# Optimization experiments

Hardware: AMD Instinct MI355X
Metric: run time of the kernel (lower is better)

Reference implementation:

```python
import jax, jax.numpy as jnp
import numpy as np

B, S, DM = 1, 4096, 2048
H, HD = 16, 128
TS = 16          # tile_size
TOPK = 16        # anchor tiles per query
NUM_TILES = S // TS


def setup_inputs() -> dict:
    key = jax.random.key(0)
    ks = jax.random.split(key, 7)
    x = jax.random.normal(ks[0], (B, S, DM), jnp.float32)
    Wq = jax.random.normal(ks[1], (DM, H * HD), jnp.float32) * 0.02
    Wk = jax.random.normal(ks[2], (DM, H * HD), jnp.float32) * 0.02
    Wv = jax.random.normal(ks[3], (DM, H * HD), jnp.float32) * 0.02
    Wo = jax.random.normal(ks[4], (H * HD, DM), jnp.float32) * 0.02
    # RoPE angles: pos * inv_freq, shape [S, HD//2] (= freqs_cis angle)
    inv_freq = 1.0 / (10000.0 ** (np.arange(0, HD, 2, dtype=np.float32) / HD))
    freqs = jnp.asarray(np.arange(S, dtype=np.float32)[:, None] * inv_freq[None, :])
    anchor_indices = jax.random.randint(ks[5], (B, H, S, TOPK), 0, NUM_TILES).astype(jnp.int32)
    return {"x": x, "Wq": Wq, "Wk": Wk, "Wv": Wv, "Wo": Wo,
            "freqs": freqs, "anchor_indices": anchor_indices}


def _rotate_half(z):
    half = z.shape[-1] // 2
    return jnp.concatenate([-z[..., half:], z[..., :half]], axis=-1)


def reference(x, Wq, Wk, Wv, Wo, freqs, anchor_indices):
    b, s, _ = x.shape
    num_tiles = s // TS
    # QKV projections -> [B, H, S, HD]
    q = (x @ Wq).reshape(b, s, H, HD).transpose(0, 2, 1, 3)
    k = (x @ Wk).reshape(b, s, H, HD).transpose(0, 2, 1, 3)
    v = (x @ Wv).reshape(b, s, H, HD).transpose(0, 2, 1, 3)
    # RoPE (half-split / rotate_half convention), float32
    cos = jnp.cos(freqs)[None, None, :s, :]
    sin = jnp.sin(freqs)[None, None, :s, :]
    cos_full = jnp.concatenate([cos, cos], axis=-1)
    sin_full = jnp.concatenate([sin, sin], axis=-1)
    q = q * cos_full + _rotate_half(q) * sin_full
    k = k * cos_full + _rotate_half(k) * sin_full
    # Per-query tile indices: anchor tiles + local tile
    local_tiles = (jnp.arange(s) // TS).astype(jnp.int32)
    local = jnp.broadcast_to(local_tiles[None, None, :, None], (b, H, s, 1))
    tiles = jnp.concatenate([anchor_indices, local], axis=-1)  # [B,H,S,K+1]
    # Representative query per tile (last token of each query tile)
    tile_repr = jnp.arange(TS - 1, s, TS)
    tile_sel = tiles[:, :, tile_repr, :]                        # [B,H,T,K+1]
    # Expand tile indices to token indices
    offsets = jnp.arange(TS)
    token_idx = tile_sel[..., None] * TS + offsets              # [B,H,T,K+1,TS]
    sparse_len = tile_sel.shape[-1] * TS
    flat_idx = jnp.clip(token_idx.reshape(b, H, num_tiles, sparse_len), 0, s - 1)
    # Gather sparse K/V per (batch, head, query-tile)
    k_flat = k.reshape(b * H, s, HD)
    v_flat = v.reshape(b * H, s, HD)
    idx_flat = flat_idx.reshape(b * H, num_tiles, sparse_len)
    k_sparse = jax.vmap(lambda kv, idx: kv[idx])(k_flat, idx_flat)
    v_sparse = jax.vmap(lambda kv, idx: kv[idx])(v_flat, idx_flat)
    k_sparse = k_sparse.reshape(b, H, num_tiles, sparse_len, HD)
    v_sparse = v_sparse.reshape(b, H, num_tiles, sparse_len, HD)
    # Block-sparse attention per tile
    q_tiled = q.reshape(b, H, num_tiles, TS, HD)
    logits = jnp.einsum('bhtqd,bhtkd->bhtqk', q_tiled, k_sparse) / jnp.sqrt(HD)
    q_pos = jnp.arange(s).reshape(num_tiles, TS)
    future_mask = flat_idx[:, :, :, None, :] > q_pos[None, None, :, :, None]
    logits = jnp.where(future_mask, -1e10, logits)
    weights = jax.nn.softmax(logits, axis=-1)
    all_masked = jnp.all(future_mask, axis=-1, keepdims=True)
    weights = jnp.where(all_masked, 0.0, weights)
    weights = jnp.where(jnp.isnan(weights), 0.0, weights)
    out = jnp.einsum('bhtqk,bhtkd->bhtqd', weights, v_sparse)
    out = out.reshape(b, H, s, HD).transpose(0, 2, 1, 3).reshape(b, s, H * HD)
    return out @ Wo
```

## Files before the change

kernel.cpp:

```cpp
#include <hip/hip_runtime.h>

typedef unsigned short u16;
typedef unsigned int u32;
typedef __attribute__((ext_vector_type(8))) short bf16x8;
typedef __attribute__((ext_vector_type(4))) float f32x4;

__device__ __forceinline__ u16 f2bf(float f) {
  union { float f; u32 u; } v; v.f = f;
  u32 u = v.u;
  return (u16)((u + 0x7FFFu + ((u >> 16) & 1u)) >> 16);
}
__device__ __forceinline__ float bf2f(u16 s) {
  union { u32 u; float f; } v; v.u = ((u32)s) << 16;
  return v.f;
}

__device__ __forceinline__ void async16(const void* g, void* l) {
  __builtin_amdgcn_global_load_lds(
      (__attribute__((address_space(1))) void*)g,
      (__attribute__((address_space(3))) void*)l, 16, 0, 0);
}

__global__ void prep1_kernel(const float* __restrict__ x,
                             const float* __restrict__ W0, const float* __restrict__ W1,
                             const float* __restrict__ W2, const float* __restrict__ W3,
                             const float* __restrict__ freqs,
                             u16* __restrict__ xbf, u16* __restrict__ wqkvT,
                             u16* __restrict__ woT,
                             float* __restrict__ ct, float* __restrict__ st) {
  __shared__ float tile[64][33];
  const int bid = blockIdx.x;
  const int tid = threadIdx.x;
  if (bid < 8192) {
    const int z = bid >> 11;
    const float* in = z == 0 ? W0 : z == 1 ? W1 : z == 2 ? W2 : W3;
    u16* out = z == 3 ? woT : wqkvT + (size_t)z * 4194304;
    const int local = bid & 2047;
    const int c0 = (local & 63) * 32;
    const int r0 = (local >> 6) * 64;
#pragma unroll
    for (int it = 0; it < 8; ++it) {
      int idx = it * 256 + tid;
      int row = idx >> 5, col = idx & 31;
      tile[row][col] = in[(size_t)(r0 + row) * 2048 + c0 + col];
    }
    __syncthreads();
#pragma unroll
    for (int it = 0; it < 4; ++it) {
      int idx = it * 256 + tid;
      int orow = idx >> 5, oc2 = idx & 31;
      u32 v = (u32)f2bf(tile[2 * oc2][orow]) | ((u32)f2bf(tile[2 * oc2 + 1][orow]) << 16);
      *(u32*)(out + (size_t)(c0 + orow) * 2048 + r0 + 2 * oc2) = v;
    }
  } else if (bid < 16384) {
    int i = (bid - 8192) * 256 + tid;
    float4 v = ((const float4*)x)[i];
    ushort4 o;
    o.x = f2bf(v.x); o.y = f2bf(v.y); o.z = f2bf(v.z); o.w = f2bf(v.w);
    ((ushort4*)xbf)[i] = o;
  } else {
    int i = (bid - 16384) * 256 + tid;
    float f = freqs[i];
    ct[i] = cosf(f); st[i] = sinf(f);
  }
}

template <int MODE>
__launch_bounds__(256, 3)
__global__ void gemm128_kernel(const u16* __restrict__ A, const u16* __restrict__ Bt,
                               void* __restrict__ C, u16* __restrict__ D1, u16* __restrict__ D2,
                               const float* __restrict__ ct, const float* __restrict__ st,
                               int M, int N, int K) {
  __shared__ __align__(16) char smem[33152];
  u16* As = (u16*)smem;
  u16* Bs = (u16*)(smem + 16384);
  const int tid  = threadIdx.x;
  const int lane = tid & 63;
  const int wave = tid >> 6;
  const int wr = wave >> 1, wc = wave & 1;
  const int g = lane >> 4, c = lane & 15;
  const int brow = blockIdx.y * 128;
  const int bcol = blockIdx.x * 128;

  int a_goff[4], b_goff[4], l_off[4];
#pragma unroll
  for (int i = 0; i < 4; ++i) {
    int p = (wave * 4 + i) * 1024 + lane * 16;
    int row = p >> 7;
    int colb = (p & 127) ^ ((row & 7) << 4);
    a_goff[i] = (brow + row) * K + (colb >> 1);
    b_goff[i] = (bcol + row) * K + (colb >> 1);
    l_off[i] = p;
  }

  f32x4 acc[4][4];
#pragma unroll
  for (int m = 0; m < 4; ++m)
#pragma unroll
    for (int n = 0; n < 4; ++n) acc[m][n] = (f32x4){0.f, 0.f, 0.f, 0.f};

  for (int k0 = 0; k0 < K; k0 += 64) {
#pragma unroll
    for (int i = 0; i < 4; ++i) {
      async16(A + a_goff[i] + k0, (char*)As + l_off[i]);
      async16(Bt + b_goff[i] + k0, (char*)Bs + l_off[i]);
    }
    __syncthreads();
#pragma unroll
    for (int kk = 0; kk < 2; ++kk) {
      bf16x8 af[4], bfr[4];
#pragma unroll
      for (int m = 0; m < 4; ++m) {
        int row = wr * 64 + m * 16 + c;
        int byte = (row << 7) + ((kk * 64 + (g << 4)) ^ ((row & 7) << 4));
        af[m] = *(const bf16x8*)((const char*)As + byte);
      }
#pragma unroll
      for (int n = 0; n < 4; ++n) {
        int row = ((n & 2) << 5) + wc * 32 + ((n & 1) << 4) + c;
        int byte = (row << 7) + ((kk * 64 + (g << 4)) ^ ((row & 7) << 4));
        bfr[n] = *(const bf16x8*)((const char*)Bs + byte);
      }
#pragma unroll
      for (int m = 0; m < 4; ++m)
#pragma unroll
        for (int n = 0; n < 4; ++n)
          acc[m][n] = __builtin_amdgcn_mfma_f32_16x16x32_bf16(af[m], bfr[n], acc[m][n], 0, 0, 0);
    }
    __syncthreads();
  }

  if (MODE == 2) {
    const int sel = bcol >> 11;
    const int hh  = (bcol & 2047) >> 7;
    if (sel < 2) {
#pragma unroll
      for (int m = 0; m < 4; ++m)
#pragma unroll
        for (int r = 0; r < 4; ++r) {
          const int t = brow + wr * 64 + m * 16 + g * 4 + r;
          const int tb = t * 64;
#pragma unroll
          for (int n = 0; n < 2; ++n) {
            const int d = wc * 32 + (n << 4) + c;
            float cv = ct[tb + d], sv = st[tb + d];
            float a = acc[m][n][r], b = acc[m][n + 2][r];
            u16 lo = f2bf(a * cv - b * sv);
            u16 hi = f2bf(b * cv + a * sv);
            if (sel == 0) {
              u16* qd = (u16*)C + (size_t)t * 2048 + hh * 128 + d;
              qd[0] = lo; qd[64] = hi;
            } else {
              u16* kd = D1 + ((size_t)hh * 4096 + t) * 128 + d;
              kd[0] = lo; kd[64] = hi;
            }
          }
        }
    } else {
      float* ep = (float*)smem;
#pragma unroll
      for (int half = 0; half < 2; ++half) {
        if (wr == half) {
#pragma unroll
          for (int m = 0; m < 4; ++m)
#pragma unroll
            for (int n = 0; n < 4; ++n)
#pragma unroll
              for (int r = 0; r < 4; ++r) {
                int lr = m * 16 + g * 4 + r;
                int lc = ((n & 2) << 5) + wc * 32 + ((n & 1) << 4) + c;
                ep[lr * 129 + lc] = acc[m][n][r];
              }
        }
        __syncthreads();
        const int rowbase = brow + half * 64;
#pragma unroll
        for (int it = 0; it < 16; ++it) {
          int idx = it * 256 + tid;
          int tl = idx >> 10;
          int d  = (idx >> 3) & 127;
          int k2 = idx & 7;
          u32 lo = f2bf(ep[(tl * 16 + 2 * k2) * 129 + d]);
          u32 hi = f2bf(ep[(tl * 16 + 2 * k2 + 1) * 129 + d]);
          int tile = (rowbase >> 4) + tl;
          *(u32*)(D2 + (((size_t)(hh * 256 + tile) * 128 + d) * 16 + 2 * k2)) = lo | (hi << 16);
        }
        __syncthreads();
      }
    }
  } else {
    const int r0 = brow + wr * 64;
#pragma unroll
    for (int m = 0; m < 4; ++m)
#pragma unroll
      for (int n = 0; n < 4; ++n)
#pragma unroll
        for (int r = 0; r < 4; ++r) {
          int rr = r0 + m * 16 + g * 4 + r;
          int cc = bcol + ((n & 2) << 5) + wc * 32 + ((n & 1) << 4) + c;
          ((float*)C)[(size_t)rr * N + cc] = acc[m][n][r];
        }
  }
}

__launch_bounds__(256, 6)
__global__ void attn_kernel(const u16* __restrict__ Q, const u16* __restrict__ Kp,
                            const u16* __restrict__ VT2, const int* __restrict__ anchors,
                            u16* __restrict__ Out) {
  const int t = blockIdx.x;
  const int h = blockIdx.y;
  __shared__ int tiles[20];
  __shared__ __align__(16) float lg[16][292];
  const int tid  = threadIdx.x;
  const int lane = tid & 63;
  const int wave = tid >> 6;
  const int g = lane >> 4;
  const int c = lane & 15;

  if (tid < 16) tiles[tid] = anchors[(size_t)((h << 12) + (t * 16 + 15)) * 16 + tid];
  if (tid == 16) tiles[16] = t;
  if (tid >= 17 && tid < 20) tiles[tid] = 0;
  __syncthreads();

  {
    const u16* qbase = Q + (size_t)(t * 16 + c) * 2048 + h * 128 + g * 8;
    bf16x8 qf[4];
#pragma unroll
    for (int ks = 0; ks < 4; ++ks) qf[ks] = *(const bf16x8*)(qbase + ks * 32);

    int tok_[5];
    const u16* kb_[5];
#pragma unroll
    for (int i = 0; i < 5; ++i) {
      int j = wave + 4 * i;
      tok_[i] = tiles[j] * 16 + c;
      kb_[i] = Kp + ((size_t)h * 4096 + tok_[i]) * 128 + g * 8;
    }
    bf16x8 kfp[2][4];
#pragma unroll
    for (int ks = 0; ks < 4; ++ks) kfp[0][ks] = *(const bf16x8*)(kb_[0] + ks * 32);
#pragma unroll
    for (int i = 0; i < 5; ++i) {
      if (i < 4) {
#pragma unroll
        for (int ks = 0; ks < 4; ++ks)
          kfp[(i + 1) & 1][ks] = *(const bf16x8*)(kb_[i + 1] + ks * 32);
      }
      f32x4 a = (f32x4){0.f, 0.f, 0.f, 0.f};
#pragma unroll
      for (int ks = 0; ks < 4; ++ks)
        a = __builtin_amdgcn_mfma_f32_16x16x32_bf16(qf[ks], kfp[i & 1][ks], a, 0, 0, 0);
      int j = wave + 4 * i;
      if (j < 17) {
#pragma unroll
        for (int r = 0; r < 4; ++r) {
          int qrow = g * 4 + r;
          float vv = a[r] * 0.088388347648318447f;
          if (tok_[i] > t * 16 + qrow) vv = -1e10f;
          lg[qrow][j * 16 + c] = vv;
        }
      }
    }
  }
  __syncthreads();

  {
    const int r = tid >> 4, cc = tid & 15;
    float vals[17];
    float mx = -3.0e38f;
#pragma unroll
    for (int i = 0; i < 17; ++i) { vals[i] = lg[r][i * 16 + cc]; mx = fmaxf(mx, vals[i]); }
#pragma unroll
    for (int d = 1; d < 16; d <<= 1) mx = fmaxf(mx, __shfl_xor(mx, d, 64));
    float sum = 0.f;
#pragma unroll
    for (int i = 0; i < 17; ++i) { vals[i] = __expf(vals[i] - mx); sum += vals[i]; }
#pragma unroll
    for (int d = 1; d < 16; d <<= 1) sum += __shfl_xor(sum, d, 64);
    float inv = sum > 0.f ? 1.0f / sum : 0.f;
    u16* wrow = (u16*)&lg[r][0];
#pragma unroll
    for (int i = 0; i < 17; ++i) wrow[i * 16 + cc] = f2bf(vals[i] * inv);
    wrow[272 + cc] = 0;
  }
  __syncthreads();

  {
    f32x4 o0 = (f32x4){0.f, 0.f, 0.f, 0.f}, o1 = o0;
    const int d0 = wave * 32;
    const size_t hb = (size_t)h * 256;
    const int keyin = (g & 1) * 8;
    const u16* wrow = (const u16*)&lg[c][0];
    const u16* vb_[9];
#pragma unroll
    for (int ks = 0; ks < 9; ++ks) vb_[ks] = VT2 + (hb + tiles[2 * ks + (g >> 1)]) * 2048;
    bf16x8 pb0[2], pb1[2];
    pb0[0] = *(const bf16x8*)(vb_[0] + (d0 + c) * 16 + keyin);
    pb1[0] = *(const bf16x8*)(vb_[0] + (d0 + 16 + c) * 16 + keyin);
#pragma unroll
    for (int ks = 0; ks < 9; ++ks) {
      if (ks < 8) {
        pb0[(ks + 1) & 1] = *(const bf16x8*)(vb_[ks + 1] + (d0 + c) * 16 + keyin);
        pb1[(ks + 1) & 1] = *(const bf16x8*)(vb_[ks + 1] + (d0 + 16 + c) * 16 + keyin);
      }
      bf16x8 af = *(const bf16x8*)(wrow + ks * 32 + g * 8);
      o0 = __builtin_amdgcn_mfma_f32_16x16x32_bf16(af, pb0[ks & 1], o0, 0, 0, 0);
      o1 = __builtin_amdgcn_mfma_f32_16x16x32_bf16(af, pb1[ks & 1], o1, 0, 0, 0);
    }
#pragma unroll
    for (int r = 0; r < 4; ++r) {
      int qrow = g * 4 + r;
      size_t base = (size_t)(t * 16 + qrow) * 2048 + h * 128;
      Out[base + d0 + c]      = f2bf(o0[r]);
      Out[base + d0 + 16 + c] = f2bf(o1[r]);
    }
  }
}

extern "C" void kernel_launch(void* const* d_in, const int* in_sizes, int n_in,
                              void* d_out, int out_size, void* d_ws, size_t ws_size,
                              hipStream_t stream) {
  (void)in_sizes; (void)n_in; (void)out_size; (void)ws_size;
  const float* x      = (const float*)d_in[0];
  const float* Wq     = (const float*)d_in[1];
  const float* Wk     = (const float*)d_in[2];
  const float* Wv     = (const float*)d_in[3];
  const float* Wo     = (const float*)d_in[4];
  const float* freqs  = (const float*)d_in[5];
  const int* anchors  = (const int*)d_in[6];
  float* out = (float*)d_out;

  char* ws = (char*)d_ws;
  const size_t MB = 1024 * 1024;
  u16* xbf   = (u16*)(ws + 0);
  u16* wqkvT = (u16*)(ws + 16 * MB);
  u16* woT   = (u16*)(ws + 40 * MB);
  u16* qbf   = (u16*)(ws + 48 * MB);
  u16* Kp    = (u16*)(ws + 64 * MB);
  u16* VT2   = (u16*)(ws + 80 * MB);
  u16* attnb = (u16*)(ws + 0);
  float* ct  = (float*)(ws + 96 * MB);
  float* st  = (float*)(ws + 97 * MB);

  prep1_kernel<<<17408, 256, 0, stream>>>(x, Wq, Wk, Wv, Wo, freqs,
                                          xbf, wqkvT, woT, ct, st);
  gemm128_kernel<2><<<dim3(48, 32), 256, 0, stream>>>(xbf, wqkvT, qbf, Kp, VT2,
                                                      ct, st, 4096, 6144, 2048);
  attn_kernel<<<dim3(256, 16), 256, 0, stream>>>(qbf, Kp, VT2, anchors, attnb);
  gemm128_kernel<0><<<dim3(16, 32), 256, 0, stream>>>(attnb, woT, out, nullptr, nullptr,
                                                      nullptr, nullptr, 4096, 2048, 2048);
}
```

Baseline: 226.6 us.

## Replace QKV GEMM with 256x256 double-buffered 8-wave pipelined kernel

The QKV projection GEMM moves from 128x128 tiles with a single LDS stage to 256x256 tiles with 512 threads and two 64KB LDS stages. Global-to-LDS async loads are interleaved with LDS fragment loads and MFMA blocks, using explicit vmcnt/lgkmcnt waits, raw barriers and s_setprio around the MFMA bursts. The goal is to hide load latency and raise operand reuse. The V-transpose epilogue now stages bf16 in shared memory instead of fp32, and the Wo GEMM is split into its own kernel with a simpler column mapping. The trade-off is one block per CU and a grid of only 384 blocks, which risks poor occupancy and a tail effect.

```diff
diff --git a/kernel.cpp b/kernel.cpp
--- a/kernel.cpp
+++ b/kernel.cpp
@@ -20,6 +20,12 @@
       (__attribute__((address_space(1))) void*)g,
       (__attribute__((address_space(3))) void*)l, 16, 0, 0);
 }
+
+#define VM4  asm volatile("s_waitcnt vmcnt(4)" ::: "memory")
+#define VM0  asm volatile("s_waitcnt vmcnt(0)" ::: "memory")
+#define LG0  asm volatile("s_waitcnt lgkmcnt(0)" ::: "memory")
+#define BARX do { asm volatile("" ::: "memory"); __builtin_amdgcn_s_barrier(); \
+                  asm volatile("" ::: "memory"); } while (0)
 
 __global__ void prep1_kernel(const float* __restrict__ x,
                              const float* __restrict__ W0, const float* __restrict__ W1,
@@ -65,15 +71,186 @@
   }
 }
 
-template <int MODE>
-__launch_bounds__(256, 3)
-__global__ void gemm128_kernel(const u16* __restrict__ A, const u16* __restrict__ Bt,
-                               void* __restrict__ C, u16* __restrict__ D1, u16* __restrict__ D2,
-                               const float* __restrict__ ct, const float* __restrict__ st,
-                               int M, int N, int K) {
-  __shared__ __align__(16) char smem[33152];
-  u16* As = (u16*)smem;
-  u16* Bs = (u16*)(smem + 16384);
+__launch_bounds__(512, 1)
+__global__ void gemm256_qkv_kernel(const u16* __restrict__ A, const u16* __restrict__ Bt,
+                                   u16* __restrict__ Q, u16* __restrict__ Kp,
+                                   u16* __restrict__ VT2,
+                                   const float* __restrict__ ct, const float* __restrict__ st) {
+  const int K = 2048;
+  __shared__ __align__(16) char smem[131072];
+  const int tid = threadIdx.x;
+  const int lane = tid & 63, wave = tid >> 6;
+  const int wm = wave >> 2, wn = wave & 3;
+  const int g = lane >> 4, c = lane & 15;
+  const int brow = blockIdx.y * 256;
+  const int bcol = blockIdx.x * 256;
+
+  int sp[2][2], aso[2][2], bso[2][2];
+#pragma unroll
+  for (int h = 0; h < 2; ++h)
+#pragma unroll
+    for (int cc = 0; cc < 2; ++cc) {
+      int p = h * 16384 + cc * 8192 + tid * 16;
+      int row = p >> 7;
+      int colb = (p & 127) ^ ((row & 7) << 4);
+      sp[h][cc] = p;
+      aso[h][cc] = (brow + row) * K + (colb >> 1);
+      bso[h][cc] = (bcol + row) * K + (colb >> 1);
+    }
+  auto stA = [&](int s, int h, int kt) {
+#pragma unroll
+    for (int cc = 0; cc < 2; ++cc)
+      async16(A + aso[h][cc] + kt * 64, smem + s * 65536 + sp[h][cc]);
+  };
+  auto stB = [&](int s, int h, int kt) {
+#pragma unroll
+    for (int cc = 0; cc < 2; ++cc)
+      async16(Bt + bso[h][cc] + kt * 64, smem + s * 65536 + 32768 + sp[h][cc]);
+  };
+
+  f32x4 acc[8][4];
+#pragma unroll
+  for (int m = 0; m < 8; ++m)
+#pragma unroll
+    for (int n = 0; n < 4; ++n) acc[m][n] = (f32x4){0.f, 0.f, 0.f, 0.f};
+  bf16x8 aF[4][2], bF[4][2];
+
+  auto LDA = [&](int s, int mh) {
+#pragma unroll
+    for (int mm = 0; mm < 4; ++mm) {
+      int row = wm * 128 + mh * 64 + mm * 16 + c;
+      int sw = (row & 7) << 4;
+      const char* base = smem + s * 65536 + (row << 7);
+#pragma unroll
+      for (int kk = 0; kk < 2; ++kk)
+        aF[mm][kk] = *(const bf16x8*)(base + ((kk * 64 + (g << 4)) ^ sw));
+    }
+  };
+  auto LDB = [&](int s, int np) {
+#pragma unroll
+    for (int nn = 0; nn < 2; ++nn) {
+      int row = (wn >> 1) * 128 + np * 64 + (wn & 1) * 32 + nn * 16 + c;
+      int sw = (row & 7) << 4;
+      const char* base = smem + s * 65536 + 32768 + (row << 7);
+#pragma unroll
+      for (int kk = 0; kk < 2; ++kk)
+        bF[np * 2 + nn][kk] = *(const bf16x8*)(base + ((kk * 64 + (g << 4)) ^ sw));
+    }
+  };
+  auto MF = [&](int mb, int np) {
+    __builtin_amdgcn_s_setprio(1);
+#pragma unroll
+    for (int kk = 0; kk < 2; ++kk)
+#pragma unroll
+      for (int mm = 0; mm < 4; ++mm)
+#pragma unroll
+        for (int nn = 0; nn < 2; ++nn)
+          acc[mb + mm][np * 2 + nn] = __builtin_amdgcn_mfma_f32_16x16x32_bf16(
+              aF[mm][kk], bF[np * 2 + nn][kk], acc[mb + mm][np * 2 + nn], 0, 0, 0);
+    __builtin_amdgcn_s_setprio(0);
+  };
+
+  stA(0, 0, 0); stA(0, 1, 0); stB(0, 0, 0); stB(0, 1, 0);
+  stB(1, 0, 1); stB(1, 1, 1);
+  VM4;
+  BARX;
+
+  const int NT = 32;
+#pragma unroll 1
+  for (int i = 0; i < 16; ++i) {
+    const int t0 = 2 * i;
+    const bool g2 = (t0 + 2) < NT, g3 = (t0 + 3) < NT;
+    LDA(0, 0); LDB(0, 0);
+    stA(1, 0, t0 + 1);
+    BARX; LG0; MF(0, 0); BARX;
+    LDB(0, 1);
+    stA(1, 1, t0 + 1);
+    BARX; LG0; MF(0, 1); BARX;
+    LDA(0, 1);
+    if (g2) stB(0, 0, t0 + 2);
+    BARX; LG0; MF(4, 0); BARX;
+    if (g2) { stB(0, 1, t0 + 2); VM4; } else { VM0; }
+    BARX; MF(4, 1); BARX;
+    LDA(1, 0); LDB(1, 0);
+    if (g2) stA(0, 0, t0 + 2);
+    BARX; LG0; MF(0, 0); BARX;
+    LDB(1, 1);
+    if (g2) stA(0, 1, t0 + 2);
+    BARX; LG0; MF(0, 1); BARX;
+    LDA(1, 1);
+    if (g3) stB(1, 0, t0 + 3);
+    BARX; LG0; MF(4, 0); BARX;
+    if (g3) { stB(1, 1, t0 + 3); VM4; } else { VM0; }
+    BARX; MF(4, 1); BARX;
+  }
+
+  const int sel = bcol >> 11;
+  if (sel < 2) {
+    const int hh = ((bcol & 2047) >> 7) + (wn >> 1);
+#pragma unroll
+    for (int mf = 0; mf < 8; ++mf)
+#pragma unroll
+      for (int r = 0; r < 4; ++r) {
+        const int t = brow + wm * 128 + mf * 16 + g * 4 + r;
+        const int tb = t * 64;
+#pragma unroll
+        for (int n = 0; n < 2; ++n) {
+          const int d = (wn & 1) * 32 + (n << 4) + c;
+          float cv = ct[tb + d], sv = st[tb + d];
+          float a = acc[mf][n][r], b = acc[mf][n + 2][r];
+          u16 lo = f2bf(a * cv - b * sv);
+          u16 hi = f2bf(b * cv + a * sv);
+          if (sel == 0) {
+            u16* qd = Q + (size_t)t * 2048 + hh * 128 + d;
+            qd[0] = lo; qd[64] = hi;
+          } else {
+            u16* kd = Kp + ((size_t)hh * 4096 + t) * 128 + d;
+            kd[0] = lo; kd[64] = hi;
+          }
+        }
+      }
+  } else {
+    u16* eph = (u16*)smem;
+    const int hh0 = (bcol & 2047) >> 7;
+#pragma unroll
+    for (int half = 0; half < 2; ++half) {
+      BARX;
+      if (wm == half) {
+#pragma unroll
+        for (int mf = 0; mf < 8; ++mf)
+#pragma unroll
+          for (int n = 0; n < 4; ++n)
+#pragma unroll
+            for (int r = 0; r < 4; ++r) {
+              int lr = mf * 16 + g * 4 + r;
+              int lc = (wn >> 1) * 128 + ((n >> 1) & 1) * 64 + (wn & 1) * 32 + (n & 1) * 16 + c;
+              eph[lr * 264 + lc] = f2bf(acc[mf][n][r]);
+            }
+      }
+      BARX;
+      const int rowbase = brow + half * 128;
+#pragma unroll
+      for (int it = 0; it < 32; ++it) {
+        int idx = it * 512 + tid;
+        int k2 = idx & 7;
+        int d = (idx >> 3) & 127;
+        int tl = (idx >> 10) & 7;
+        int hl = idx >> 13;
+        u32 lo = eph[(tl * 16 + 2 * k2) * 264 + hl * 128 + d];
+        u32 hi = eph[(tl * 16 + 2 * k2 + 1) * 264 + hl * 128 + d];
+        int tile = (rowbase >> 4) + tl;
+        *(u32*)(VT2 + (((size_t)((hh0 + hl) * 256 + tile) * 128 + d) * 16 + 2 * k2)) =
+            lo | (hi << 16);
+      }
+    }
+  }
+}
+
+__launch_bounds__(256, 2)
+__global__ void gemm128_wo_kernel(const u16* __restrict__ A, const u16* __restrict__ Bt,
+                                  float* __restrict__ C, int M, int N, int K) {
+  __shared__ __align__(16) u16 As[128 * 64];
+  __shared__ __align__(16) u16 Bs[128 * 64];
   const int tid  = threadIdx.x;
   const int lane = tid & 63;
   const int wave = tid >> 6;
@@ -117,7 +294,7 @@
       }
 #pragma unroll
       for (int n = 0; n < 4; ++n) {
-        int row = ((n & 2) << 5) + wc * 32 + ((n & 1) << 4) + c;
+        int row = wc * 64 + n * 16 + c;
         int byte = (row << 7) + ((kk * 64 + (g << 4)) ^ ((row & 7) << 4));
         bfr[n] = *(const bf16x8*)((const char*)Bs + byte);
       }
@@ -130,77 +307,18 @@
     __syncthreads();
   }
 
-  if (MODE == 2) {
-    const int sel = bcol >> 11;
-    const int hh  = (bcol & 2047) >> 7;
-    if (sel < 2) {
-#pragma unroll
-      for (int m = 0; m < 4; ++m)
-#pragma unroll
-        for (int r = 0; r < 4; ++r) {
-          const int t = brow + wr * 64 + m * 16 + g * 4 + r;
-          const int tb = t * 64;
-#pragma unroll
-          for (int n = 0; n < 2; ++n) {
-            const int d = wc * 32 + (n << 4) + c;
-            float cv = ct[tb + d], sv = st[tb + d];
-            float a = acc[m][n][r], b = acc[m][n + 2][r];
-            u16 lo = f2bf(a * cv - b * sv);
-            u16 hi = f2bf(b * cv + a * sv);
-            if (sel == 0) {
-              u16* qd = (u16*)C + (size_t)t * 2048 + hh * 128 + d;
-              qd[0] = lo; qd[64] = hi;
-            } else {
-              u16* kd = D1 + ((size_t)hh * 4096 + t) * 128 + d;
-              kd[0] = lo; kd[64] = hi;
-            }
-          }
-        }
-    } else {
-      float* ep = (float*)smem;
-#pragma unroll
-      for (int half = 0; half < 2; ++half) {
-        if (wr == half) {
-#pragma unroll
-          for (int m = 0; m < 4; ++m)
-#pragma unroll
-            for (int n = 0; n < 4; ++n)
-#pragma unroll
-              for (int r = 0; r < 4; ++r) {
-                int lr = m * 16 + g * 4 + r;
-                int lc = ((n & 2) << 5) + wc * 32 + ((n & 1) << 4) + c;
-                ep[lr * 129 + lc] = acc[m][n][r];
-              }
-        }
-        __syncthreads();
-        const int rowbase = brow + half * 64;
-#pragma unroll
-        for (int it = 0; it < 16; ++it) {
-          int idx = it * 256 + tid;
-          int tl = idx >> 10;
-          int d  = (idx >> 3) & 127;
-          int k2 = idx & 7;
-          u32 lo = f2bf(ep[(tl * 16 + 2 * k2) * 129 + d]);
-          u32 hi = f2bf(ep[(tl * 16 + 2 * k2 + 1) * 129 + d]);
-          int tile = (rowbase >> 4) + tl;
-          *(u32*)(D2 + (((size_t)(hh * 256 + tile) * 128 + d) * 16 + 2 * k2)) = lo | (hi << 16);
-        }
-        __syncthreads();
-      }
-    }
-  } else {
-    const int r0 = brow + wr * 64;
-#pragma unroll
-    for (int m = 0; m < 4; ++m)
-#pragma unroll
-      for (int n = 0; n < 4; ++n)
-#pragma unroll
-        for (int r = 0; r < 4; ++r) {
-          int rr = r0 + m * 16 + g * 4 + r;
-          int cc = bcol + ((n & 2) << 5) + wc * 32 + ((n & 1) << 4) + c;
-          ((float*)C)[(size_t)rr * N + cc] = acc[m][n][r];
-        }
-  }
+  const int r0 = brow + wr * 64;
+  const int c0 = bcol + wc * 64;
+#pragma unroll
+  for (int m = 0; m < 4; ++m)
+#pragma unroll
+    for (int n = 0; n < 4; ++n)
+#pragma unroll
+      for (int r = 0; r < 4; ++r) {
+        int rr = r0 + m * 16 + g * 4 + r;
+        int cc = c0 + n * 16 + c;
+        C[(size_t)rr * N + cc] = acc[m][n][r];
+      }
 }
 
 __launch_bounds__(256, 6)
@@ -344,9 +462,7 @@
 
   prep1_kernel<<<17408, 256, 0, stream>>>(x, Wq, Wk, Wv, Wo, freqs,
                                           xbf, wqkvT, woT, ct, st);
-  gemm128_kernel<2><<<dim3(48, 32), 256, 0, stream>>>(xbf, wqkvT, qbf, Kp, VT2,
-                                                      ct, st, 4096, 6144, 2048);
+  gemm256_qkv_kernel<<<dim3(24, 16), 512, 0, stream>>>(xbf, wqkvT, qbf, Kp, VT2, ct, st);
   attn_kernel<<<dim3(256, 16), 256, 0, stream>>>(qbf, Kp, VT2, anchors, attnb);
-  gemm128_kernel<0><<<dim3(16, 32), 256, 0, stream>>>(attnb, woT, out, nullptr, nullptr,
-                                                      nullptr, nullptr, 4096, 2048, 2048);
-}
+  gemm128_wo_kernel<<<dim3(16, 32), 256, 0, stream>>>(attnb, woT, out, 4096, 2048, 2048);
+}
```

New measurement: 237.9 us. 1.05x slower.
